# Kernel optimization log

Hardware: AMD Instinct MI355X
Metric: run time of the kernel (lower is better)

## Reference

```python
import jax, jax.numpy as jnp
import numpy as np

# ---- DMP constants (from DMPParameters with N=5, tau=1, dt=1/(T*l), Dof=9, a_z=25) ----
N_BASIS = 5
T_STEPS = 10
L_SUB = 10
DIM = 9                      # len(state_index)
TAU = 1.0
DT = TAU / (T_STEPS * L_SUB)            # 0.01
TIME_STEPS = int(round(TAU / DT)) + 1   # 101
A_X = 1.0
A_Z = 25.0
B_Z = A_Z / 4.0
_c_np = np.exp(-A_X * np.linspace(0.0, 1.0, N_BASIS))
C = jnp.asarray(_c_np, dtype=jnp.float32)                          # rbf centers
H = jnp.asarray(N_BASIS ** 1.5 / _c_np / A_X, dtype=jnp.float32)   # rbf widths (sigma2)


def _integrate(w, y0, dy0, goal):
    """Euler integration of the DMP dynamical system.
    w: (R, N) basis weights; y0, dy0, goal: (R,) with R = batch*DIM.
    Returns Y: (R, TIME_STEPS) positions."""
    scale = goal - y0  # fixed forcing-term scaling

    def step(carry, _):
        y, z, x = carry
        x = x + (-A_X * x / TAU) * DT                  # canonical system
        psi = jnp.exp(-H * (x - C) ** 2)               # (N,) gaussian rbf
        fx = (w @ psi) * x * scale / jnp.sum(psi)      # (R,) forcing term
        dz = (A_Z * (B_Z * (goal - y) - z) + fx) / TAU
        dy = z / TAU
        y = y + dy * DT
        z = z + dz * DT
        return (y, z, x), y

    z0 = dy0 * TAU
    _, ys = jax.lax.scan(step, (y0, z0, jnp.float32(1.0)), None, length=TIME_STEPS - 1)
    # prepend initial position, transpose to (R, TIME_STEPS)
    return jnp.concatenate([y0[None, :], ys], axis=0).T


def setup_inputs():
    key = jax.random.key(0)
    ks = jax.random.split(key, 4)
    B, D_IN, HID = 16384, 128, 2048
    out_size = DIM * (N_BASIS + 1)  # 54 = N*dim + dim
    return {
        "input": jax.random.normal(ks[0], (B, D_IN), jnp.float32),
        "W0": jax.random.normal(ks[1], (HID, D_IN), jnp.float32) / np.sqrt(D_IN),
        "b0": jnp.full((HID,), 0.1, jnp.float32),
        "W1": jax.random.normal(ks[2], (HID, HID), jnp.float32) / np.sqrt(HID),
        "b1": jnp.full((HID,), 0.1, jnp.float32),
        "Wl": jax.random.normal(ks[3], (out_size, HID), jnp.float32) / np.sqrt(HID),
        "bl": jnp.zeros((out_size,), jnp.float32),
    }


def reference(input, W0, b0, W1, b1, Wl, bl):
    B = input.shape[0]
    # MLP backbone with tanh hidden activation
    h = jnp.tanh(input @ W0.T + b0)
    h = jnp.tanh(h @ W1.T + b1)
    out = (h @ Wl.T + bl) * 100.0                          # (B, DIM*(N+1))
    # split DMP parameters: goal then basis weights
    goal = out[:, :DIM].reshape(-1)                        # (B*DIM,)
    w = out[:, DIM:DIM * (N_BASIS + 1)].reshape(-1, N_BASIS)  # (B*DIM, N)
    y0 = input[:, 7:16].reshape(-1)                        # state_index
    dy0 = input[:, 22:31].reshape(-1)                      # vel_index
    Y = _integrate(w, y0, dy0, goal)                       # (B*DIM, 101)
    y = Y.reshape(B, DIM, TIME_STEPS)[:, :, ::L_SUB]       # (B, DIM, T+1)
    return y[:, :, 1:] - y[:, :, :-1]                      # (B, DIM, T)
```

## Files before the change

kernel.cpp:

```cpp
#include <hip/hip_runtime.h>
#include <hip/hip_fp16.h>
#include <math.h>

typedef _Float16 f16;
typedef _Float16 f16x8 __attribute__((ext_vector_type(8)));
typedef _Float16 f16x4v __attribute__((ext_vector_type(4)));
typedef float f32x4 __attribute__((ext_vector_type(4)));

#define B_SZ 16384
#define D_INP 128
#define HID 2048
#define DIMS 9
#define OUTC 54
#define OUTP 64
#define NZ3 4

__device__ __forceinline__ void load_lds16(const f16* g, f16* l) {
    __builtin_amdgcn_global_load_lds(
        (__attribute__((address_space(1))) void*)(g),
        (__attribute__((address_space(3))) void*)(l),
        16, 0, 0);
}

__device__ __forceinline__ float fast_tanh(float x) {
    float e = __builtin_amdgcn_exp2f(2.885390081777927f * x);
    return 1.0f - 2.0f * __builtin_amdgcn_rcpf(e + 1.0f);
}

#define N4_W0  (HID * D_INP / 4)
#define N4_W1  (HID * HID / 4)
#define N4_WL  (OUTP * HID / 4)
__global__ __launch_bounds__(256) void cvt_fused_kernel(
    const float* __restrict__ W0, const float* __restrict__ W1,
    const float* __restrict__ Wl,
    f16* __restrict__ w0q, f16* __restrict__ w1p, f16* __restrict__ wlq)
{
    int i = blockIdx.x * 256 + threadIdx.x;
    if (i < N4_W0) {
        float4 v = ((const float4*)W0)[i];
        f16x4v o; o.x = (f16)v.x; o.y = (f16)v.y; o.z = (f16)v.z; o.w = (f16)v.w;
        ((f16x4v*)w0q)[i] = o;
    } else if (i < N4_W0 + N4_W1) {
        int j = i - N4_W0;
        int n = j >> 9;
        int k = (j & 511) << 2;
        float4 v = ((const float4*)W1)[j];
        f16x4v o; o.x = (f16)v.x; o.y = (f16)v.y; o.z = (f16)v.z; o.w = (f16)v.w;
        int blk   = ((n >> 4) << 6) | (k >> 5);
        int lanep = (((k >> 3) & 3) << 4) | (n & 15);
        int off   = (blk << 9) + (lanep << 3) + (k & 7);
        *(f16x4v*)(w1p + off) = o;
    } else {
        int j = i - N4_W0 - N4_W1;
        int e0 = j * 4, row = e0 >> 11;
        f16x4v o;
        if (row < OUTC) {
            float4 v = ((const float4*)Wl)[j];
            o.x = (f16)v.x; o.y = (f16)v.y; o.z = (f16)v.z; o.w = (f16)v.w;
        } else {
            o.x = (f16)0.f; o.y = (f16)0.f; o.z = (f16)0.f; o.w = (f16)0.f;
        }
        ((f16x4v*)wlq)[j] = o;
    }
}

template <int BN, int EPI>
__global__ __launch_bounds__(256, 2) void gemm_nt(
    const f16* __restrict__ A, const f16* __restrict__ Bm,
    const float* __restrict__ bias, void* __restrict__ Cout,
    int M, int N, int K, int bias_n)
{
    constexpr int BM = 128, BK = 64;
    constexpr int NI = BN / 32;
    __shared__ __align__(16) f16 sa[BM * BK];
    __shared__ __align__(16) f16 sb[BN * BK];

    const int tid  = threadIdx.x;
    const int lane = tid & 63;
    const int wave = tid >> 6;
    const int wm = wave >> 1, wn = wave & 1;

    const int flat = blockIdx.x + blockIdx.y * gridDim.x;
    const int gsz  = 8 * gridDim.y;
    const int grp  = flat / gsz;
    const int rem  = flat - grp * gsz;
    const int m0 = (grp * 8 + (rem & 7)) * BM;
    const int n0 = (rem >> 3) * BN;

    const int k_len = K / gridDim.z;
    const int k_beg = blockIdx.z * k_len;
    const int k_end = k_beg + k_len;

    f32x4 acc[4][NI];
    #pragma unroll
    for (int i = 0; i < 4; ++i)
        #pragma unroll
        for (int j = 0; j < NI; ++j) acc[i][j] = (f32x4){0.f, 0.f, 0.f, 0.f};

    const int r8 = lane >> 3;
    const int cg = (((lane & 7) ^ r8) << 3);

    for (int k0 = k_beg; k0 < k_end; k0 += BK) {
        #pragma unroll
        for (int c = 0; c < (BM * BK * 2) / 4096; ++c) {
            int o = c * 4096 + wave * 1024;
            const f16* gp = A + (size_t)(m0 + (o >> 7) + r8) * K + k0 + cg;
            load_lds16(gp, (f16*)((char*)sa + o));
        }
        #pragma unroll
        for (int c = 0; c < (BN * BK * 2) / 4096; ++c) {
            int o = c * 4096 + wave * 1024;
            const f16* gp = Bm + (size_t)(n0 + (o >> 7) + r8) * K + k0 + cg;
            load_lds16(gp, (f16*)((char*)sb + o));
        }
        __syncthreads();

        #pragma unroll
        for (int kc = 0; kc < 2; ++kc) {
            f16x8 af[4], bf[NI];
            #pragma unroll
            for (int mi = 0; mi < 4; ++mi) {
                int ar = wm * 64 + mi * 16 + (lane & 15);
                af[mi] = *(const f16x8*)&sa[ar * 64 + ((((kc << 2) | (lane >> 4)) ^ (ar & 7)) << 3)];
            }
            #pragma unroll
            for (int ni = 0; ni < NI; ++ni) {
                int br = wn * (BN / 2) + ni * 16 + (lane & 15);
                bf[ni] = *(const f16x8*)&sb[br * 64 + ((((kc << 2) | (lane >> 4)) ^ (br & 7)) << 3)];
            }
            #pragma unroll
            for (int mi = 0; mi < 4; ++mi)
                #pragma unroll
                for (int ni = 0; ni < NI; ++ni)
                    acc[mi][ni] = __builtin_amdgcn_mfma_f32_16x16x32_f16(af[mi], bf[ni], acc[mi][ni], 0, 0, 0);
        }
        __syncthreads();
    }

    const int crow0 = m0 + wm * 64 + (lane >> 4) * 4;
    const int ccol0 = n0 + wn * (BN / 2) + (lane & 15);
    if (EPI == 0) {
        f16* C = (f16*)Cout;
        #pragma unroll
        for (int mi = 0; mi < 4; ++mi)
            #pragma unroll
            for (int ni = 0; ni < NI; ++ni) {
                int col = ccol0 + ni * 16;
                float bv = bias[col];
                #pragma unroll
                for (int r2 = 0; r2 < 4; ++r2) {
                    float v = fast_tanh(acc[mi][ni][r2] + bv);
                    C[(size_t)(crow0 + mi * 16 + r2) * N + col] = (f16)v;
                }
            }
    } else {
        float* C = (float*)Cout + (size_t)blockIdx.z * M * N;
        #pragma unroll
        for (int mi = 0; mi < 4; ++mi)
            #pragma unroll
            for (int ni = 0; ni < NI; ++ni) {
                int col = ccol0 + ni * 16;
                float bv = (blockIdx.z == 0 && col < bias_n) ? bias[col] * 100.0f : 0.0f;
                #pragma unroll
                for (int r2 = 0; r2 < 4; ++r2) {
                    float v = acc[mi][ni][r2] * 100.0f + bv;
                    C[(size_t)(crow0 + mi * 16 + r2) * N + col] = v;
                }
            }
    }
}

__global__ __launch_bounds__(256, 2) void gemm2_bpacked(
    const f16* __restrict__ A, const f16* __restrict__ Bp,
    const float* __restrict__ bias, f16* __restrict__ C)
{
    constexpr int BM = 128, BK = 64, NI = 4;
    constexpr int N = HID, K = HID;
    __shared__ __align__(16) f16 sa[BM * BK];

    const int tid  = threadIdx.x;
    const int lane = tid & 63;
    const int wave = tid >> 6;
    const int wm = wave >> 1, wn = wave & 1;

    const int flat = blockIdx.x + blockIdx.y * gridDim.x;
    const int gsz  = 8 * gridDim.y;
    const int grp  = flat / gsz;
    const int rem  = flat - grp * gsz;
    const int m0 = (grp * 8 + (rem & 7)) * BM;
    const int n0 = (rem >> 3) * 128;

    f32x4 acc[4][NI];
    #pragma unroll
    for (int i = 0; i < 4; ++i)
        #pragma unroll
        for (int j = 0; j < NI; ++j) acc[i][j] = (f32x4){0.f, 0.f, 0.f, 0.f};

    const int r8 = lane >> 3;
    const int cg = (((lane & 7) ^ r8) << 3);

    const f16* bbase = Bp + (((size_t)(n0 >> 4) + wn * 4) << 15) + (lane << 3);

    for (int k0 = 0; k0 < K; k0 += BK) {
        #pragma unroll
        for (int c = 0; c < 4; ++c) {
            int o = c * 4096 + wave * 1024;
            const f16* gp = A + (size_t)(m0 + (o >> 7) + r8) * K + k0 + cg;
            load_lds16(gp, (f16*)((char*)sa + o));
        }
        f16x8 bf[2][NI];
        const int kb = k0 >> 5;
        #pragma unroll
        for (int kc = 0; kc < 2; ++kc)
            #pragma unroll
            for (int ni = 0; ni < NI; ++ni)
                bf[kc][ni] = *(const f16x8*)(bbase + (((ni << 6) + kb + kc) << 9));
        __syncthreads();

        #pragma unroll
        for (int kc = 0; kc < 2; ++kc) {
            f16x8 af[4];
            #pragma unroll
            for (int mi = 0; mi < 4; ++mi) {
                int ar = wm * 64 + mi * 16 + (lane & 15);
                af[mi] = *(const f16x8*)&sa[ar * 64 + ((((kc << 2) | (lane >> 4)) ^ (ar & 7)) << 3)];
            }
            #pragma unroll
            for (int mi = 0; mi < 4; ++mi)
                #pragma unroll
                for (int ni = 0; ni < NI; ++ni)
                    acc[mi][ni] = __builtin_amdgcn_mfma_f32_16x16x32_f16(af[mi], bf[kc][ni], acc[mi][ni], 0, 0, 0);
        }
        __syncthreads();
    }

    const int crow0 = m0 + wm * 64 + (lane >> 4) * 4;
    const int ccol0 = n0 + wn * 64 + (lane & 15);
    #pragma unroll
    for (int mi = 0; mi < 4; ++mi)
        #pragma unroll
        for (int ni = 0; ni < NI; ++ni) {
            int col = ccol0 + ni * 16;
            float bv = bias[col];
            #pragma unroll
            for (int r2 = 0; r2 < 4; ++r2) {
                float v = fast_tanh(acc[mi][ni][r2] + bv);
                C[(size_t)(crow0 + mi * 16 + r2) * N + col] = (f16)v;
            }
        }
}

__global__ __launch_bounds__(256, 2) void gemm1_f32a(
    const float* __restrict__ A, const f16* __restrict__ Bm,
    const float* __restrict__ bias, f16* __restrict__ C)
{
    constexpr int BM = 128, BK = 64, BN = 128, NI = 4;
    constexpr int N = HID, K = D_INP;
    __shared__ __align__(16) f16 sa[BM * BK];
    __shared__ __align__(16) f16 sb[BN * BK];

    const int tid  = threadIdx.x;
    const int lane = tid & 63;
    const int wave = tid >> 6;
    const int wm = wave >> 1, wn = wave & 1;

    const int flat = blockIdx.x + blockIdx.y * gridDim.x;
    const int gsz  = 8 * gridDim.y;
    const int grp  = flat / gsz;
    const int rem  = flat - grp * gsz;
    const int m0 = (grp * 8 + (rem & 7)) * BM;
    const int n0 = (rem >> 3) * BN;

    f32x4 acc[4][NI];
    #pragma unroll
    for (int i = 0; i < 4; ++i)
        #pragma unroll
        for (int j = 0; j < NI; ++j) acc[i][j] = (f32x4){0.f, 0.f, 0.f, 0.f};

    const int r8 = lane >> 3;
    const int cg = (((lane & 7) ^ r8) << 3);

    for (int k0 = 0; k0 < K; k0 += BK) {
        #pragma unroll
        for (int c = 0; c < (BM * BK * 2) / 4096; ++c) {
            int o = c * 4096 + wave * 1024;
            const float* gp = A + (size_t)(m0 + (o >> 7) + r8) * K + k0 + cg;
            float4 v0 = *(const float4*)gp;
            float4 v1 = *(const float4*)(gp + 4);
            f16x8 h;
            h[0] = (f16)v0.x; h[1] = (f16)v0.y; h[2] = (f16)v0.z; h[3] = (f16)v0.w;
            h[4] = (f16)v1.x; h[5] = (f16)v1.y; h[6] = (f16)v1.z; h[7] = (f16)v1.w;
            *(f16x8*)((char*)sa + o + (lane << 4)) = h;
        }
        #pragma unroll
        for (int c = 0; c < (BN * BK * 2) / 4096; ++c) {
            int o = c * 4096 + wave * 1024;
            const f16* gp = Bm + (size_t)(n0 + (o >> 7) + r8) * K + k0 + cg;
            load_lds16(gp, (f16*)((char*)sb + o));
        }
        __syncthreads();

        #pragma unroll
        for (int kc = 0; kc < 2; ++kc) {
            f16x8 af[4], bf[NI];
            #pragma unroll
            for (int mi = 0; mi < 4; ++mi) {
                int ar = wm * 64 + mi * 16 + (lane & 15);
                af[mi] = *(const f16x8*)&sa[ar * 64 + ((((kc << 2) | (lane >> 4)) ^ (ar & 7)) << 3)];
            }
            #pragma unroll
            for (int ni = 0; ni < NI; ++ni) {
                int br = wn * 64 + ni * 16 + (lane & 15);
                bf[ni] = *(const f16x8*)&sb[br * 64 + ((((kc << 2) | (lane >> 4)) ^ (br & 7)) << 3)];
            }
            #pragma unroll
            for (int mi = 0; mi < 4; ++mi)
                #pragma unroll
                for (int ni = 0; ni < NI; ++ni)
                    acc[mi][ni] = __builtin_amdgcn_mfma_f32_16x16x32_f16(af[mi], bf[ni], acc[mi][ni], 0, 0, 0);
        }
        __syncthreads();
    }

    const int crow0 = m0 + wm * 64 + (lane >> 4) * 4;
    const int ccol0 = n0 + wn * 64 + (lane & 15);
    #pragma unroll
    for (int mi = 0; mi < 4; ++mi)
        #pragma unroll
        for (int ni = 0; ni < NI; ++ni) {
            int col = ccol0 + ni * 16;
            float bv = bias[col];
            #pragma unroll
            for (int r2 = 0; r2 < 4; ++r2) {
                float v = fast_tanh(acc[mi][ni][r2] + bv);
                C[(size_t)(crow0 + mi * 16 + r2) * N + col] = (f16)v;
            }
        }
}

__global__ __launch_bounds__(256) void integrate_kernel(
    const float* __restrict__ out3p, const float* __restrict__ input,
    float* __restrict__ out)
{
    __shared__ float g[500];
    {
        int k = threadIdx.x;
        if (k < 100) {
            float x = expf(-0.010050335853501441f * (float)(k + 1));
            float psi[5], ssum = 0.0f;
            #pragma unroll
            for (int n = 0; n < 5; ++n) {
                float c = expf(-0.25f * (float)n);
                float h = 11.180339887498949f / c;
                float dx = x - c;
                psi[n] = expf(-h * dx * dx);
                ssum += psi[n];
            }
            float inv = x / ssum;
            #pragma unroll
            for (int n = 0; n < 5; ++n) g[k * 5 + n] = psi[n] * inv;
        }
    }
    __syncthreads();

    int r = blockIdx.x * 256 + threadIdx.x;
    int b = r / DIMS, d = r - b * DIMS;

    float goal = 0.f, w0 = 0.f, w1 = 0.f, w2 = 0.f, w3 = 0.f, w4 = 0.f;
    #pragma unroll
    for (int z = 0; z < NZ3; ++z) {
        const float* ob = out3p + (size_t)z * B_SZ * OUTP + (size_t)b * OUTP;
        goal += ob[d];
        w0 += ob[DIMS + d * 5 + 0];
        w1 += ob[DIMS + d * 5 + 1];
        w2 += ob[DIMS + d * 5 + 2];
        w3 += ob[DIMS + d * 5 + 3];
        w4 += ob[DIMS + d * 5 + 4];
    }

    float y = input[(size_t)b * D_INP + 7 + d];
    float z = input[(size_t)b * D_INP + 22 + d];
    const float scale = goal - y;

    float prev = y;
    float* op = out + (size_t)b * (DIMS * 10) + d * 10;
    int j = 0;
    for (int k = 0; k < 100; ++k) {
        const float* gk = &g[k * 5];
        float fx = scale * (w0 * gk[0] + w1 * gk[1] + w2 * gk[2] + w3 * gk[3] + w4 * gk[4]);
        float dz = 25.0f * (6.25f * (goal - y) - z) + fx;
        y = y + z * 0.01f;
        z = z + dz * 0.01f;
        if ((k % 10) == 9) { op[j] = y - prev; prev = y; ++j; }
    }
}

extern "C" void kernel_launch(void* const* d_in, const int* in_sizes, int n_in,
                              void* d_out, int out_size, void* d_ws, size_t ws_size,
                              hipStream_t stream) {
    (void)in_sizes; (void)n_in; (void)out_size; (void)ws_size;
    const float* input = (const float*)d_in[0];
    const float* W0 = (const float*)d_in[1];
    const float* b0 = (const float*)d_in[2];
    const float* W1 = (const float*)d_in[3];
    const float* b1 = (const float*)d_in[4];
    const float* Wl = (const float*)d_in[5];
    const float* bl = (const float*)d_in[6];
    float* out = (float*)d_out;

    f16* w0q = (f16*)d_ws;
    f16* w1p = w0q + (size_t)HID * D_INP;
    f16* wlq = w1p + (size_t)HID * HID;
    f16* h1  = wlq + (size_t)OUTP * HID;
    f16* h2  = h1 + (size_t)B_SZ * HID;
    float* out3p = (float*)h1;

    int n4_total = N4_W0 + N4_W1 + N4_WL;
    cvt_fused_kernel<<<(n4_total + 255) / 256, 256, 0, stream>>>(
        W0, W1, Wl, w0q, w1p, wlq);

    gemm1_f32a<<<dim3(B_SZ / 128, HID / 128), 256, 0, stream>>>(
        input, w0q, b0, h1);
    gemm2_bpacked<<<dim3(B_SZ / 128, HID / 128), 256, 0, stream>>>(
        h1, w1p, b1, h2);
    gemm_nt<64, 1><<<dim3(B_SZ / 128, 1, NZ3), 256, 0, stream>>>(
        h2, wlq, bl, (void*)out3p, B_SZ, OUTP, HID, OUTC);

    integrate_kernel<<<B_SZ * DIMS / 256, 256, 0, stream>>>(out3p, input, out);
}
```

Baseline: 273.2 us.

## Double-buffer LDS tiles for both operands in the hidden-layer GEMM

The hidden-layer GEMM drops the pre-packed W1 layout read straight from global memory into registers. It now stages both the A and B tiles through LDS using async global-to-LDS loads, double-buffered so the next K tile loads while the current one is computed. The weight conversion kernel becomes a plain row-major fp16 cast for W1. This aims to hide global latency behind MFMA work. In exchange it doubles LDS use (64KB per block), which may limit occupancy, and adds LDS reads for B.

Result: no change. 277.3 us (+1.5%).

```diff
diff --git a/kernel.cpp b/kernel.cpp
--- a/kernel.cpp
+++ b/kernel.cpp
@@ -33,25 +33,14 @@
 __global__ __launch_bounds__(256) void cvt_fused_kernel(
     const float* __restrict__ W0, const float* __restrict__ W1,
     const float* __restrict__ Wl,
-    f16* __restrict__ w0q, f16* __restrict__ w1p, f16* __restrict__ wlq)
+    f16* __restrict__ w0q, f16* __restrict__ w1q, f16* __restrict__ wlq)
 {
     int i = blockIdx.x * 256 + threadIdx.x;
-    if (i < N4_W0) {
-        float4 v = ((const float4*)W0)[i];
-        f16x4v o; o.x = (f16)v.x; o.y = (f16)v.y; o.z = (f16)v.z; o.w = (f16)v.w;
-        ((f16x4v*)w0q)[i] = o;
-    } else if (i < N4_W0 + N4_W1) {
-        int j = i - N4_W0;
-        int n = j >> 9;
-        int k = (j & 511) << 2;
-        float4 v = ((const float4*)W1)[j];
-        f16x4v o; o.x = (f16)v.x; o.y = (f16)v.y; o.z = (f16)v.z; o.w = (f16)v.w;
-        int blk   = ((n >> 4) << 6) | (k >> 5);
-        int lanep = (((k >> 3) & 3) << 4) | (n & 15);
-        int off   = (blk << 9) + (lanep << 3) + (k & 7);
-        *(f16x4v*)(w1p + off) = o;
-    } else {
-        int j = i - N4_W0 - N4_W1;
+    const float* s; f16* d; int j;
+    if (i < N4_W0) { s = W0; d = w0q; j = i; }
+    else if (i < N4_W0 + N4_W1) { s = W1; d = w1q; j = i - N4_W0; }
+    else {
+        j = i - N4_W0 - N4_W1;
         int e0 = j * 4, row = e0 >> 11;
         f16x4v o;
         if (row < OUTC) {
@@ -61,7 +50,12 @@
             o.x = (f16)0.f; o.y = (f16)0.f; o.z = (f16)0.f; o.w = (f16)0.f;
         }
         ((f16x4v*)wlq)[j] = o;
-    }
+        return;
+    }
+    float4 v = ((const float4*)s)[j];
+    f16x4v o;
+    o.x = (f16)v.x; o.y = (f16)v.y; o.z = (f16)v.z; o.w = (f16)v.w;
+    ((f16x4v*)d)[j] = o;
 }
 
 template <int BN, int EPI>
@@ -170,13 +164,14 @@
     }
 }
 
-__global__ __launch_bounds__(256, 2) void gemm2_bpacked(
-    const f16* __restrict__ A, const f16* __restrict__ Bp,
+__global__ __launch_bounds__(256, 2) void gemm2_dbuf(
+    const f16* __restrict__ A, const f16* __restrict__ Bm,
     const float* __restrict__ bias, f16* __restrict__ C)
 {
-    constexpr int BM = 128, BK = 64, NI = 4;
+    constexpr int BM = 128, BN = 128, BK = 64, NI = 4;
     constexpr int N = HID, K = HID;
-    __shared__ __align__(16) f16 sa[BM * BK];
+    __shared__ __align__(16) f16 sa[2][BM * BK];
+    __shared__ __align__(16) f16 sb[2][BN * BK];
 
     const int tid  = threadIdx.x;
     const int lane = tid & 63;
@@ -188,7 +183,7 @@
     const int grp  = flat / gsz;
     const int rem  = flat - grp * gsz;
     const int m0 = (grp * 8 + (rem & 7)) * BM;
-    const int n0 = (rem >> 3) * 128;
+    const int n0 = (rem >> 3) * BN;
 
     f32x4 acc[4][NI];
     #pragma unroll
@@ -199,39 +194,50 @@
     const int r8 = lane >> 3;
     const int cg = (((lane & 7) ^ r8) << 3);
 
-    const f16* bbase = Bp + (((size_t)(n0 >> 4) + wn * 4) << 15) + (lane << 3);
-
+    #pragma unroll
+    for (int c = 0; c < 4; ++c) {
+        int o = c * 4096 + wave * 1024;
+        load_lds16(A + (size_t)(m0 + (o >> 7) + r8) * K + cg, (f16*)((char*)sa[0] + o));
+        load_lds16(Bm + (size_t)(n0 + (o >> 7) + r8) * K + cg, (f16*)((char*)sb[0] + o));
+    }
+    __syncthreads();
+
+    int cur = 0;
     for (int k0 = 0; k0 < K; k0 += BK) {
-        #pragma unroll
-        for (int c = 0; c < 4; ++c) {
-            int o = c * 4096 + wave * 1024;
-            const f16* gp = A + (size_t)(m0 + (o >> 7) + r8) * K + k0 + cg;
-            load_lds16(gp, (f16*)((char*)sa + o));
-        }
-        f16x8 bf[2][NI];
-        const int kb = k0 >> 5;
-        #pragma unroll
-        for (int kc = 0; kc < 2; ++kc)
-            #pragma unroll
-            for (int ni = 0; ni < NI; ++ni)
-                bf[kc][ni] = *(const f16x8*)(bbase + (((ni << 6) + kb + kc) << 9));
-        __syncthreads();
-
+        if (k0 + BK < K) {
+            int nxt = cur ^ 1;
+            #pragma unroll
+            for (int c = 0; c < 4; ++c) {
+                int o = c * 4096 + wave * 1024;
+                load_lds16(A + (size_t)(m0 + (o >> 7) + r8) * K + (k0 + BK) + cg,
+                           (f16*)((char*)sa[nxt] + o));
+                load_lds16(Bm + (size_t)(n0 + (o >> 7) + r8) * K + (k0 + BK) + cg,
+                           (f16*)((char*)sb[nxt] + o));
+            }
+        }
+        const f16* pa = sa[cur];
+        const f16* pb = sb[cur];
         #pragma unroll
         for (int kc = 0; kc < 2; ++kc) {
-            f16x8 af[4];
+            f16x8 af[4], bf[NI];
             #pragma unroll
             for (int mi = 0; mi < 4; ++mi) {
                 int ar = wm * 64 + mi * 16 + (lane & 15);
-                af[mi] = *(const f16x8*)&sa[ar * 64 + ((((kc << 2) | (lane >> 4)) ^ (ar & 7)) << 3)];
+                af[mi] = *(const f16x8*)&pa[ar * 64 + ((((kc << 2) | (lane >> 4)) ^ (ar & 7)) << 3)];
+            }
+            #pragma unroll
+            for (int ni = 0; ni < NI; ++ni) {
+                int br = wn * 64 + ni * 16 + (lane & 15);
+                bf[ni] = *(const f16x8*)&pb[br * 64 + ((((kc << 2) | (lane >> 4)) ^ (br & 7)) << 3)];
             }
             #pragma unroll
             for (int mi = 0; mi < 4; ++mi)
                 #pragma unroll
                 for (int ni = 0; ni < NI; ++ni)
-                    acc[mi][ni] = __builtin_amdgcn_mfma_f32_16x16x32_f16(af[mi], bf[kc][ni], acc[mi][ni], 0, 0, 0);
+                    acc[mi][ni] = __builtin_amdgcn_mfma_f32_16x16x32_f16(af[mi], bf[ni], acc[mi][ni], 0, 0, 0);
         }
         __syncthreads();
+        cur ^= 1;
     }
 
     const int crow0 = m0 + wm * 64 + (lane >> 4) * 4;
@@ -409,20 +415,20 @@
     float* out = (float*)d_out;
 
     f16* w0q = (f16*)d_ws;
-    f16* w1p = w0q + (size_t)HID * D_INP;
-    f16* wlq = w1p + (size_t)HID * HID;
+    f16* w1q = w0q + (size_t)HID * D_INP;
+    f16* wlq = w1q + (size_t)HID * HID;
     f16* h1  = wlq + (size_t)OUTP * HID;
     f16* h2  = h1 + (size_t)B_SZ * HID;
     float* out3p = (float*)h1;
 
     int n4_total = N4_W0 + N4_W1 + N4_WL;
     cvt_fused_kernel<<<(n4_total + 255) / 256, 256, 0, stream>>>(
-        W0, W1, Wl, w0q, w1p, wlq);
+        W0, W1, Wl, w0q, w1q, wlq);
 
     gemm1_f32a<<<dim3(B_SZ / 128, HID / 128), 256, 0, stream>>>(
         input, w0q, b0, h1);
-    gemm2_bpacked<<<dim3(B_SZ / 128, HID / 128), 256, 0, stream>>>(
-        h1, w1p, b1, h2);
+    gemm2_dbuf<<<dim3(B_SZ / 128, HID / 128), 256, 0, stream>>>(
+        h1, w1q, b1, h2);
     gemm_nt<64, 1><<<dim3(B_SZ / 128, 1, NZ3), 256, 0, stream>>>(
         h2, wlq, bl, (void*)out3p, B_SZ, OUTP, HID, OUTC);
 
```
